# Performance work log

Hardware: AMD Instinct MI355X
Metric: run time of the kernel (lower is better)

The kernel has to match this reference:

```python
import jax, jax.numpy as jnp
import numpy as np

N, E, B = 65536, 131072, 2048
NUM_FEATURES, EDGE_FEATURES, DIM = 75, 16, 64


def setup_inputs() -> dict:
    key = jax.random.key(0)
    ks = jax.random.split(key, 24)

    def p(i, shape, scale=0.05):
        return jax.random.normal(ks[i], shape, dtype=jnp.float32) * scale

    return {
        "node_features": p(0, (N, NUM_FEATURES), 1.0),
        "edge_features": p(1, (E, EDGE_FEATURES), 1.0),
        "edge_index": jax.random.randint(ks[2], (2, E), 0, N),
        "graph_index": jnp.sort(jax.random.randint(ks[3], (N,), 0, B)),
        "lin0_w": p(4, (NUM_FEATURES, DIM)),
        "lin0_b": p(5, (DIM,)),
        "mlp_w1": p(6, (EDGE_FEATURES, 128)),
        "mlp_b1": p(7, (128,)),
        "mlp_w2": p(8, (128, DIM * DIM)),
        "mlp_b2": p(9, (DIM * DIM,)),
        "conv_bias": p(10, (DIM,)),
        "gru_w_ih": p(11, (3 * DIM, DIM)),
        "gru_w_hh": p(12, (3 * DIM, DIM)),
        "gru_b_ih": p(13, (3 * DIM,)),
        "gru_b_hh": p(14, (3 * DIM,)),
        "lstm_w_ih": p(15, (4 * DIM, 2 * DIM)),
        "lstm_w_hh": p(16, (4 * DIM, DIM)),
        "lstm_b_ih": p(17, (4 * DIM,)),
        "lstm_b_hh": p(18, (4 * DIM,)),
    }


def reference(node_features, edge_features, edge_index, graph_index,
              lin0_w, lin0_b, mlp_w1, mlp_b1, mlp_w2, mlp_b2, conv_bias,
              gru_w_ih, gru_w_hh, gru_b_ih, gru_b_hh,
              lstm_w_ih, lstm_w_hh, lstm_b_ih, lstm_b_hh):
    n = node_features.shape[0]
    d = DIM
    src, dst = edge_index[0], edge_index[1]

    # edge-conditioned weights (identical every iteration in the original loop)
    ew = jnp.maximum(edge_features @ mlp_w1 + mlp_b1, 0.0) @ mlp_w2 + mlp_b2
    W = ew.reshape(-1, d, d)  # [E, d, d]
    counts = jnp.maximum(
        jax.ops.segment_sum(jnp.ones(src.shape[0], jnp.float32), dst, num_segments=n), 1.0)

    out = jnp.maximum(node_features @ lin0_w + lin0_b, 0.0)
    h = out
    for _ in range(3):
        # NNConv: gather src, per-edge matmul, scatter-mean to dst
        msg = jnp.einsum('ed,edf->ef', out[src], W)
        agg = jax.ops.segment_sum(msg, dst, num_segments=n) / counts[:, None]
        m = jnp.maximum(agg + conv_bias, 0.0)
        # GRU step (seq len 1)
        gi = m @ gru_w_ih.T + gru_b_ih
        gh = h @ gru_w_hh.T + gru_b_hh
        r = jax.nn.sigmoid(gi[:, :d] + gh[:, :d])
        z = jax.nn.sigmoid(gi[:, d:2 * d] + gh[:, d:2 * d])
        nn_ = jnp.tanh(gi[:, 2 * d:] + r * gh[:, 2 * d:])
        h = (1.0 - z) * nn_ + z * h
        out = h
    feat_map = out

    # Set2Set pooling, 3 processing steps
    q_star = jnp.zeros((B, 2 * d), jnp.float32)
    hs = jnp.zeros((B, d), jnp.float32)
    cs = jnp.zeros((B, d), jnp.float32)
    for _ in range(3):
        gates = q_star @ lstm_w_ih.T + lstm_b_ih + hs @ lstm_w_hh.T + lstm_b_hh
        i_g = jax.nn.sigmoid(gates[:, :d])
        f_g = jax.nn.sigmoid(gates[:, d:2 * d])
        g_g = jnp.tanh(gates[:, 2 * d:3 * d])
        o_g = jax.nn.sigmoid(gates[:, 3 * d:])
        cs = f_g * cs + i_g * g_g
        hs = o_g * jnp.tanh(cs)
        q = hs  # [B, d]
        e = jnp.sum(out * q[graph_index], axis=-1)  # [N]
        e = e - jax.ops.segment_max(e, graph_index, num_segments=B)[graph_index]
        a = jnp.exp(e)
        a = a / (jax.ops.segment_sum(a, graph_index, num_segments=B)[graph_index] + 1e-16)
        rvec = jax.ops.segment_sum(a[:, None] * out, graph_index, num_segments=B)
        q_star = jnp.concatenate([q, rvec], axis=-1)
    return (q_star, feat_map)
```

## Files before the change

### kernel.cpp

```cpp
#include <hip/hip_runtime.h>
#include <hip/hip_bf16.h>

#define GN 65536
#define GE 131072
#define GB 2048

typedef __attribute__((ext_vector_type(8))) short short8;
typedef __attribute__((ext_vector_type(4))) float floatx4;

static __device__ __forceinline__ float sigm(float x) { return 1.0f / (1.0f + __expf(-x)); }
static __device__ __forceinline__ float bf2f(unsigned short u) {
    union { unsigned int i; float f; } v; v.i = ((unsigned int)u) << 16; return v.f;
}
static __device__ __forceinline__ int geti(const void* p, long long i, int f64) {
    return f64 ? (int)((const long long*)p)[i] : ((const int*)p)[i];
}

struct DetectArgs { const void* src[17]; int nhalf[17]; int fi[17]; };
__global__ void k_detect(DetectArgs a, const unsigned int* __restrict__ pe,
                         const unsigned int* __restrict__ pg,
                         int* __restrict__ flags, int* __restrict__ flagE,
                         int* __restrict__ flagG) {
    __shared__ unsigned int sA[256], sB[256];
    if (blockIdx.x >= 17) {
        const unsigned int* p = (blockIdx.x == 17) ? pe : pg;
        const long long nwords = (blockIdx.x == 17) ? (long long)2 * GE : (long long)GN;
        const long long lim = nwords < 16384 ? nwords : 16384;
        unsigned int acc = 0;
        for (long long w = 1 + 2 * (long long)threadIdx.x; w < lim; w += 512) acc |= p[w];
        sA[threadIdx.x] = acc;
        __syncthreads();
        for (int st = 128; st > 0; st >>= 1) {
            if (threadIdx.x < st) sA[threadIdx.x] |= sA[threadIdx.x + st];
            __syncthreads();
        }
        if (threadIdx.x == 0) *((blockIdx.x == 17) ? flagE : flagG) = (sA[0] == 0u) ? 1 : 0;
        return;
    }
    const unsigned short* p = (const unsigned short*)a.src[blockIdx.x];
    const int n0 = a.nhalf[blockIdx.x];
    const int n = n0 < 16384 ? n0 : 16384;
    unsigned int any = 0, orEven = 0;
    for (int i = threadIdx.x; i < n; i += 256) {
        const unsigned short u = p[i];
        const float av = fabsf(bf2f(u));
        if (!(av <= 1e6f)) any = 1u;
        if ((i & 1) == 0) orEven |= u;
    }
    sA[threadIdx.x] = any; sB[threadIdx.x] = orEven;
    __syncthreads();
    for (int s = 128; s > 0; s >>= 1) {
        if (threadIdx.x < s) {
            sA[threadIdx.x] |= sA[threadIdx.x + s];
            sB[threadIdx.x] |= sB[threadIdx.x + s];
        }
        __syncthreads();
    }
    if (threadIdx.x == 0) flags[a.fi[blockIdx.x]] = (sA[0] || sB[0] == 0u) ? 1 : 0;
}

struct CvtArgs { const void* src[15]; float* dst[15]; int n[15]; int fi[15]; int pre[16]; };
__global__ void k_cvt_all(CvtArgs a, const int* __restrict__ flags) {
    const int b = blockIdx.x;
    int t = 0;
    while (t < 14 && b >= a.pre[t + 1]) ++t;
    const int i = (b - a.pre[t]) * 256 + threadIdx.x;
    if (i >= a.n[t]) return;
    const int f = flags[a.fi[t]];
    a.dst[t][i] = f ? ((const float*)a.src[t])[i] : bf2f(((const unsigned short*)a.src[t])[i]);
}

__global__ __launch_bounds__(256) void k_t2(const void* __restrict__ src,
                                            __hip_bfloat16* __restrict__ w2P,
                                            const int* __restrict__ flag) {
    const int tid8 = blockIdx.x * 256 + threadIdx.x;
    const int quad = tid8 & 3, lr = (tid8 >> 2) & 15, rb = (tid8 >> 6) & 7,
              kk = (tid8 >> 9) & 3, t = tid8 >> 11;
    const int n = t * 128 + rb * 16 + lr;
    const int k0 = kk * 32 + quad * 8;
    const int isf32 = *flag;
    short8 v;
    #pragma unroll
    for (int j = 0; j < 8; ++j) {
        const size_t si = (size_t)(k0 + j) * 4096 + n;
        const float f = isf32 ? ((const float*)src)[si] : bf2f(((const unsigned short*)src)[si]);
        const __hip_bfloat16 b = __float2bfloat16(f);
        v[j] = *(const short*)&b;
    }
    *(short8*)(w2P + (size_t)tid8 * 8) = v;
}

__global__ void k_gpack2(const float* __restrict__ w_ih, const float* __restrict__ w_hh,
                         __hip_bfloat16* __restrict__ gwp) {
    const int t = blockIdx.x * 256 + threadIdx.x;
    if (t >= 3072) return;
    const int lane = t & 63;
    const int kk = (t >> 6) & 1;
    const int nb = (t >> 7) % 12;
    const int mat = t / 1536;
    const float* W = mat ? w_hh : w_ih;
    const int c = nb * 16 + (lane & 15);
    const int k0 = kk * 32 + (lane >> 4) * 8;
    short8 hi, lo;
    #pragma unroll
    for (int j = 0; j < 8; ++j) {
        const float v = W[c * 64 + k0 + j];
        const __hip_bfloat16 bh = __float2bfloat16(v);
        hi[j] = *(const short*)&bh;
        const __hip_bfloat16 bl = __float2bfloat16(v - __bfloat162float(bh));
        lo[j] = *(const short*)&bl;
    }
    const size_t base = (size_t)(((mat * 12 + nb) * 2 + kk) * 2);
    *(short8*)(gwp + (base + 0) * 512 + lane * 8) = hi;
    *(short8*)(gwp + (base + 1) * 512 + lane * 8) = lo;
}

__global__ void k_counts(const void* __restrict__ eidx, const int* __restrict__ fi64,
                         float* __restrict__ counts, int E_) {
    int e = blockIdx.x * 256 + threadIdx.x;
    if (e < E_) atomicAdd(&counts[geti(eidx, (long long)E_ + e, *fi64)], 1.0f);
}

__global__ void k_rowptr(const void* __restrict__ gi, const int* __restrict__ fi64,
                         int* __restrict__ rowptr, int N_, int B_) {
    int g = blockIdx.x * 256 + threadIdx.x;
    if (g > B_) return;
    const int f64 = *fi64;
    int lo = 0, hi = N_;
    while (lo < hi) { int mid = (lo + hi) >> 1; if (geti(gi, mid, f64) < g) lo = mid + 1; else hi = mid; }
    rowptr[g] = lo;
}

__global__ __launch_bounds__(256) void k_lin0(const void* __restrict__ nf_raw,
                                              const float* __restrict__ w,
                                              const float* __restrict__ b,
                                              float* __restrict__ out,
                                              const int* __restrict__ flag) {
    const int ln = threadIdx.x >> 6;
    const int d = threadIdx.x & 63;
    const int n = blockIdx.x * 4 + ln;
    const int isf32 = *flag;
    __shared__ float s_nf[4][76];
    const size_t base = (size_t)n * 75;
    s_nf[ln][d] = isf32 ? ((const float*)nf_raw)[base + d] : bf2f(((const unsigned short*)nf_raw)[base + d]);
    if (d < 11) s_nf[ln][64 + d] = isf32 ? ((const float*)nf_raw)[base + 64 + d]
                                         : bf2f(((const unsigned short*)nf_raw)[base + 64 + d]);
    __syncthreads();
    float acc = b[d];
    #pragma unroll
    for (int i = 0; i < 75; ++i) acc += s_nf[ln][i] * w[i * 64 + d];
    out[(size_t)n * 64 + d] = fmaxf(acc, 0.0f);
}

__global__ __launch_bounds__(256) void k1_h1(const void* __restrict__ ef_raw,
                                             const float* __restrict__ w1,
                                             const float* __restrict__ b1,
                                             __hip_bfloat16* __restrict__ h1P,
                                             const int* __restrict__ flag) {
    const int le = threadIdx.x >> 7;
    const int j = threadIdx.x & 127;
    const int e = blockIdx.x * 2 + le;
    const int isf32 = *flag;
    __shared__ float efs[2][16];
    if (j < 16) {
        const size_t idx = (size_t)e * 16 + j;
        efs[le][j] = isf32 ? ((const float*)ef_raw)[idx] : bf2f(((const unsigned short*)ef_raw)[idx]);
    }
    __syncthreads();
    float acc = b1[j];
    #pragma unroll
    for (int i = 0; i < 16; ++i) acc += efs[le][i] * w1[i * 128 + j];
    const int eb = e >> 6, er = e & 63, rb = er >> 4, lre = er & 15;
    const int kk = j >> 5, qd = (j >> 3) & 3, jj = j & 7;
    h1P[(size_t)eb * 8192 + (kk * 4 + rb) * 512 + (qd * 16 + lre) * 8 + jj] =
        __float2bfloat16(fmaxf(acc, 0.0f));
}

__global__ __launch_bounds__(256) void k23_fused(const __hip_bfloat16* __restrict__ h1P,
                                                 const __hip_bfloat16* __restrict__ w2P,
                                                 const float* __restrict__ b2,
                                                 const float* __restrict__ out,
                                                 const void* __restrict__ eidx,
                                                 const int* __restrict__ fi64,
                                                 float* __restrict__ agg) {
    __shared__ __align__(16) __hip_bfloat16 As[64 * 128];
    __shared__ float yT[64][65];
    __shared__ int sdx[64];
    const int tid = threadIdx.x;
    const int e0 = blockIdx.x * 64;
    const int f64 = *fi64;

    const int wave = tid >> 6, lane = tid & 63;
    const int wn = wave * 32;
    const int lr = lane & 15, quad = lane >> 4;

    if (tid < 64) sdx[tid] = geti(eidx, (long long)GE + e0 + tid, f64);
    {
        const short8* s8 = (const short8*)(h1P + (size_t)blockIdx.x * 8192);
        short8* d8 = (short8*)As;
        #pragma unroll
        for (int i = 0; i < 4; ++i) d8[i * 256 + tid] = s8[i * 256 + tid];
    }
    {
        const int e = tid >> 2, d0 = (tid & 3) * 16;
        const int s = geti(eidx, e0 + e, f64);
        const float* srow = out + (size_t)s * 64 + d0;
        #pragma unroll
        for (int j = 0; j < 4; ++j) {
            float4 v = *(const float4*)(srow + j * 4);
            yT[d0 + j * 4 + 0][e] = v.x;
            yT[d0 + j * 4 + 1][e] = v.y;
            yT[d0 + j * 4 + 2][e] = v.z;
            yT[d0 + j * 4 + 3][e] = v.w;
        }
    }
    __syncthreads();

    const int lin = (lr * 4 + quad) * 8;
    const char* Ab = (const char*)As + lane * 16;
    float msum[4][2][4] = {};

#define K23_LOADB(dst, tt)                                                      \
    _Pragma("unroll")                                                           \
    for (int kk = 0; kk < 4; ++kk) {                                            \
        _Pragma("unroll")                                                       \
        for (int nt = 0; nt < 2; ++nt) {                                        \
            const int g = ((tt) * 4 + kk) * 8 + (wn >> 4) + nt;                 \
            dst[kk][nt] = *(const short8*)(w2P + (size_t)g * 512 + lin);        \
        }                                                                       \
    }                                                                           \
    __builtin_amdgcn_sched_barrier(0);

#define K23_BODY(tt, buf) {                                                     \
    const int n0 = (tt) * 128;                                                  \
    const int dcur = (n0 + wn) >> 6;                                            \
    const float b2v0 = b2[n0 + wn + lr];                                        \
    const float b2v1 = b2[n0 + wn + 16 + lr];                                   \
    floatx4 acc[4][2] = {};                                                     \
    _Pragma("unroll")                                                           \
    for (int kk = 0; kk < 4; ++kk) {                                            \
        short8 a0, a1, a2, a3;                                                  \
        a0 = *(const short8*)(Ab + kk * 4096 + 0 * 1024);                       \
        a1 = *(const short8*)(Ab + kk * 4096 + 1 * 1024);                       \
        a2 = *(const short8*)(Ab + kk * 4096 + 2 * 1024);                       \
        a3 = *(const short8*)(Ab + kk * 4096 + 3 * 1024);                       \
        __builtin_amdgcn_s_setprio(1);                                          \
        acc[0][0] = __builtin_amdgcn_mfma_f32_16x16x32_bf16(a0, buf[kk][0], acc[0][0], 0, 0, 0); \
        acc[0][1] = __builtin_amdgcn_mfma_f32_16x16x32_bf16(a0, buf[kk][1], acc[0][1], 0, 0, 0); \
        acc[1][0] = __builtin_amdgcn_mfma_f32_16x16x32_bf16(a1, buf[kk][0], acc[1][0], 0, 0, 0); \
        acc[1][1] = __builtin_amdgcn_mfma_f32_16x16x32_bf16(a1, buf[kk][1], acc[1][1], 0, 0, 0); \
        acc[2][0] = __builtin_amdgcn_mfma_f32_16x16x32_bf16(a2, buf[kk][0], acc[2][0], 0, 0, 0); \
        acc[2][1] = __builtin_amdgcn_mfma_f32_16x16x32_bf16(a2, buf[kk][1], acc[2][1], 0, 0, 0); \
        acc[3][0] = __builtin_amdgcn_mfma_f32_16x16x32_bf16(a3, buf[kk][0], acc[3][0], 0, 0, 0); \
        acc[3][1] = __builtin_amdgcn_mfma_f32_16x16x32_bf16(a3, buf[kk][1], acc[3][1], 0, 0, 0); \
        __builtin_amdgcn_s_setprio(0);                                          \
    }                                                                           \
    _Pragma("unroll")                                                           \
    for (int mt = 0; mt < 4; ++mt) {                                            \
        _Pragma("unroll")                                                       \
        for (int r = 0; r < 4; ++r) {                                           \
            const float yv = yT[dcur][mt * 16 + quad * 4 + r];                  \
            msum[mt][0][r] = fmaf(yv, acc[mt][0][r] + b2v0, msum[mt][0][r]);    \
            msum[mt][1][r] = fmaf(yv, acc[mt][1][r] + b2v1, msum[mt][1][r]);    \
        }                                                                       \
    }                                                                           \
}

    short8 bA[4][2], bB[4][2];
    K23_LOADB(bA, 0)
    #pragma unroll 1
    for (int t = 0; t < 32; t += 2) {
        K23_LOADB(bB, t + 1)
        K23_BODY(t, bA)
        if (t + 2 < 32) { K23_LOADB(bA, t + 2) }
        K23_BODY(t + 1, bB)
    }
#undef K23_LOADB
#undef K23_BODY

    __syncthreads();
    float* mg = (float*)As;
    const int fb = (wn & 32);
    if (wave < 2) {
        #pragma unroll
        for (int mt = 0; mt < 4; ++mt)
            #pragma unroll
            for (int r = 0; r < 4; ++r)
                #pragma unroll
                for (int nt = 0; nt < 2; ++nt)
                    mg[(mt * 16 + quad * 4 + r) * 64 + fb + nt * 16 + lr] = msum[mt][nt][r];
    }
    __syncthreads();
    if (wave >= 2) {
        #pragma unroll
        for (int mt = 0; mt < 4; ++mt)
            #pragma unroll
            for (int r = 0; r < 4; ++r)
                #pragma unroll
                for (int nt = 0; nt < 2; ++nt)
                    mg[(mt * 16 + quad * 4 + r) * 64 + fb + nt * 16 + lr] += msum[mt][nt][r];
    }
    __syncthreads();
    #pragma unroll
    for (int i = 0; i < 16; ++i) {
        const int o = i * 256 + tid;
        const int row = o >> 6, col = o & 63;
        atomicAdd(&agg[(size_t)sdx[row] * 64 + col], mg[o]);
    }
}

__global__ __launch_bounds__(256) void k4_gru(const float* __restrict__ agg,
                                              const float* __restrict__ counts,
                                              const float* __restrict__ cbias,
                                              const __hip_bfloat16* __restrict__ gwp,
                                              const float* __restrict__ b_ih,
                                              const float* __restrict__ b_hh,
                                              float* __restrict__ out) {
    const int wv = threadIdx.x >> 6, lane = threadIdx.x & 63;
    const int lr = lane & 15, quad = lane >> 4;
    const int wnb0 = blockIdx.x * 64 + wv * 16;
    const int node = wnb0 + lr;

    const float rcnt = 1.0f / fmaxf(counts[node], 1.0f);
    const float* ap = agg + (size_t)node * 64;
    const float* hp = out + (size_t)node * 64;
    short8 am[2], ah[2];
    #pragma unroll
    for (int kk = 0; kk < 2; ++kk) {
        const int k0 = kk * 32 + quad * 8;
        #pragma unroll
        for (int j = 0; j < 8; ++j) {
            const float mv = fmaxf(ap[k0 + j] * rcnt + cbias[k0 + j], 0.0f);
            const __hip_bfloat16 mb = __float2bfloat16(mv);
            am[kk][j] = *(const short*)&mb;
            const __hip_bfloat16 hb = __float2bfloat16(hp[k0 + j]);
            ah[kk][j] = *(const short*)&hb;
        }
    }

    floatx4 ai[12] = {}, ahh[12] = {};
    #pragma unroll
    for (int nb = 0; nb < 12; ++nb) {
        #pragma unroll
        for (int kk = 0; kk < 2; ++kk) {
            #pragma unroll
            for (int part = 0; part < 2; ++part) {
                const short8 bi = *(const short8*)(gwp + (size_t)(((0 * 12 + nb) * 2 + kk) * 2 + part) * 512 + lane * 8);
                ai[nb] = __builtin_amdgcn_mfma_f32_16x16x32_bf16(am[kk], bi, ai[nb], 0, 0, 0);
                const short8 bh = *(const short8*)(gwp + (size_t)(((1 * 12 + nb) * 2 + kk) * 2 + part) * 512 + lane * 8);
                ahh[nb] = __builtin_amdgcn_mfma_f32_16x16x32_bf16(ah[kk], bh, ahh[nb], 0, 0, 0);
            }
        }
    }

    #pragma unroll
    for (int f = 0; f < 4; ++f) {
        const int d = f * 16 + lr;
        const float bir = b_ih[d],       bhr = b_hh[d];
        const float biz = b_ih[64 + d],  bhz = b_hh[64 + d];
        const float bin = b_ih[128 + d], bhn = b_hh[128 + d];
        #pragma unroll
        for (int r = 0; r < 4; ++r) {
            const int row = wnb0 + quad * 4 + r;
            const float rr = sigm(ai[f][r] + bir + ahh[f][r] + bhr);
            const float zz = sigm(ai[f + 4][r] + biz + ahh[f + 4][r] + bhz);
            const float nn = tanhf(ai[f + 8][r] + bin + rr * (ahh[f + 8][r] + bhn));
            const float hd = out[(size_t)row * 64 + d];
            out[(size_t)row * 64 + d] = (1.0f - zz) * nn + zz * hd;
        }
    }
}

__global__ __launch_bounds__(256) void k5_fused(float* __restrict__ qstar,
                                                const float* __restrict__ w_ih,
                                                const float* __restrict__ w_hh,
                                                const float* __restrict__ b_ih,
                                                const float* __restrict__ b_hh,
                                                const float* __restrict__ out,
                                                const int* __restrict__ rowptr) {
    const int g = blockIdx.x;
    const int j = threadIdx.x;
    __shared__ float qs[128], hv[64], gates[256];
    __shared__ float smw[4], sSw[4], srw[4][64];
    if (j < 128) qs[j] = 0.0f;
    if (j < 64) hv[j] = 0.0f;
    float creg = 0.0f;
    const int wv = j >> 6, lane = j & 63;
    const int start = rowptr[g], end = rowptr[g + 1];
    const float bsum = b_ih[j] + b_hh[j];

    for (int step = 0; step < 3; ++step) {
        __syncthreads();
        float acc = bsum;
        for (int k4 = 0; k4 < 128; k4 += 4) {
            float4 v = *(const float4*)(w_ih + (size_t)j * 128 + k4);
            const float* pv = (const float*)&v;
            #pragma unroll
            for (int t = 0; t < 4; ++t) acc += qs[k4 + t] * pv[t];
        }
        for (int k4 = 0; k4 < 64; k4 += 4) {
            float4 v = *(const float4*)(w_hh + (size_t)j * 64 + k4);
            const float* pv = (const float*)&v;
            #pragma unroll
            for (int t = 0; t < 4; ++t) acc += hv[k4 + t] * pv[t];
        }
        gates[j] = acc;
        __syncthreads();
        if (j < 64) {
            const float ig = sigm(gates[j]);
            const float fg = sigm(gates[64 + j]);
            const float gg = tanhf(gates[128 + j]);
            const float og = sigm(gates[192 + j]);
            creg = fg * creg + ig * gg;
            const float h = og * tanhf(creg);
            hv[j] = h;
            qs[j] = h;
        }
        __syncthreads();
        const float q = hv[lane];
        float m = -3.4e38f, S = 0.0f, racc = 0.0f;
        for (int n = start + wv; n < end; n += 4) {
            const float ov = out[(size_t)n * 64 + lane];
            float p = ov * q;
            #pragma unroll
            for (int off = 1; off < 64; off <<= 1) p += __shfl_xor(p, off);
            if (p > m) {
                const float sc = __expf(m - p);
                S = S * sc + 1.0f;
                racc = racc * sc + ov;
                m = p;
            } else {
                const float w = __expf(p - m);
                S += w;
                racc += w * ov;
            }
        }
        if (lane == 0) { smw[wv] = m; sSw[wv] = S; }
        srw[wv][lane] = racc;
        __syncthreads();
        if (wv == 0) {
            const float mstar = fmaxf(fmaxf(smw[0], smw[1]), fmaxf(smw[2], smw[3]));
            float Ssum = 0.0f, rsum = 0.0f;
            #pragma unroll
            for (int i = 0; i < 4; ++i) {
                const float sc = __expf(smw[i] - mstar);
                Ssum += sSw[i] * sc;
                rsum += srw[i][lane] * sc;
            }
            qs[64 + lane] = rsum / (Ssum + 1e-16f);
        }
    }
    __syncthreads();
    if (j < 128) qstar[(size_t)g * 128 + j] = qs[j];
}

__global__ void k_out(const float* __restrict__ qstar, const float* __restrict__ outb,
                      float* __restrict__ dst, int nq, int nfeat, int out_n) {
    int i = blockIdx.x * 256 + threadIdx.x;
    if (i >= out_n) return;
    float v = 0.0f;
    if (i < nq) v = qstar[i];
    else if (i - nq < nfeat) v = outb[i - nq];
    dst[i] = v;
}

extern "C" void kernel_launch(void* const* d_in, const int* in_sizes, int n_in,
                              void* d_out, int out_size, void* d_ws, size_t ws_size,
                              hipStream_t stream) {
    constexpr int N = GN, E = GE, B = GB;

    char* ws = (char*)d_ws;
    size_t off = 0;
    auto alloc = [&](size_t bytes) { size_t o = off; off = (off + bytes + 255) & ~(size_t)255; return o; };

    int*   fl     = (int*)  (ws + alloc(19 * 4));
    int*   flagE  = (int*)  (ws + alloc(256));
    int*   flagG  = (int*)  (ws + alloc(256));
    float* counts = (float*)(ws + alloc((size_t)N * 4));
    int*   rowptr = (int*)  (ws + alloc((size_t)(B + 1) * 4));
    float* outbuf = (float*)(ws + alloc((size_t)N * 64 * 4));
    float* agg    = (float*)(ws + alloc((size_t)N * 64 * 4));
    float* qstar  = (float*)(ws + alloc((size_t)B * 128 * 4));
    __hip_bfloat16* h1  = (__hip_bfloat16*)(ws + alloc((size_t)E * 128 * 2));
    __hip_bfloat16* w2P = (__hip_bfloat16*)(ws + alloc((size_t)4096 * 128 * 2));
    __hip_bfloat16* gwp = (__hip_bfloat16*)(ws + alloc((size_t)2 * 12 * 2 * 2 * 512 * 2));

    const int fidx[15]  = {4, 5, 6, 7, 8, 9, 10, 11, 12, 13, 14, 15, 16, 17, 18};
    const int fsize[15] = {75 * 64, 64, 16 * 128, 128, 128 * 4096, 4096, 64,
                           192 * 64, 192 * 64, 192, 192, 256 * 128, 256 * 64, 256, 256};
    float* F[19] = {};
    for (int t = 0; t < 15; ++t) F[fidx[t]] = (float*)(ws + alloc((size_t)fsize[t] * 4));

    DetectArgs da;
    da.src[0] = d_in[0]; da.nhalf[0] = N * 75; da.fi[0] = 0;
    da.src[1] = d_in[1]; da.nhalf[1] = E * 16; da.fi[1] = 1;
    for (int t = 0; t < 15; ++t) { da.src[2 + t] = d_in[fidx[t]]; da.nhalf[2 + t] = fsize[t]; da.fi[2 + t] = fidx[t]; }
    k_detect<<<19, 256, 0, stream>>>(da, (const unsigned int*)d_in[2],
                                     (const unsigned int*)d_in[3], fl, flagE, flagG);

    CvtArgs ca;
    int pre = 0;
    for (int t = 0; t < 15; ++t) {
        ca.src[t] = d_in[fidx[t]]; ca.dst[t] = F[fidx[t]]; ca.n[t] = fsize[t]; ca.fi[t] = fidx[t];
        ca.pre[t] = pre; pre += (fsize[t] + 255) / 256;
    }
    ca.pre[15] = pre;
    k_cvt_all<<<pre, 256, 0, stream>>>(ca, fl);
    k_t2<<<256, 256, 0, stream>>>(d_in[8], w2P, fl + 8);
    k_gpack2<<<12, 256, 0, stream>>>(F[11], F[12], gwp);

    hipMemsetAsync(counts, 0, (size_t)N * 4, stream);
    hipMemsetAsync(qstar, 0, (size_t)B * 128 * 4, stream);

    k_counts<<<E / 256, 256, 0, stream>>>(d_in[2], flagE, counts, E);
    k_rowptr<<<(B + 1 + 255) / 256, 256, 0, stream>>>(d_in[3], flagG, rowptr, N, B);
    k_lin0<<<N / 4, 256, 0, stream>>>(d_in[0], F[4], F[5], outbuf, fl + 0);
    k1_h1<<<E / 2, 256, 0, stream>>>(d_in[1], F[6], F[7], h1, fl + 1);

    for (int it = 0; it < 3; ++it) {
        hipMemsetAsync(agg, 0, (size_t)N * 64 * 4, stream);
        k23_fused<<<E / 64, 256, 0, stream>>>(h1, w2P, F[9], outbuf, d_in[2], flagE, agg);
        k4_gru<<<N / 64, 256, 0, stream>>>(agg, counts, F[10], gwp, F[13], F[14], outbuf);
    }
    k5_fused<<<B, 256, 0, stream>>>(qstar, F[15], F[16], F[17], F[18], outbuf, rowptr);
    k_out<<<(out_size + 255) / 256, 256, 0, stream>>>(qstar, outbuf, (float*)d_out,
                                                      B * 128, N * 64, out_size);
}
```

Before: 970.9 us.

## Merge setup kernels, batch lin0/h1 per block, fold agg zeroing into GRU

Combines the counts and rowptr kernels into one launch. lin0 now processes 16 nodes per block with the weight matrix staged in shared memory, and h1 processes 16 edges per block with weight columns held in registers. The per-iteration agg memset is replaced by having the GRU kernel zero agg after reading it, and k23_fused gets a launch-bounds occupancy hint. The conversion of mlp_w2 is removed from the generic conversion pass, since it is handled by the transpose kernel. Together these aim to cut launch count, redundant weight loads and memset traffic, at the cost of GRU doing extra stores.

```diff
diff --git a/kernel.cpp b/kernel.cpp
--- a/kernel.cpp
+++ b/kernel.cpp
@@ -115,18 +115,18 @@
     *(short8*)(gwp + (base + 1) * 512 + lane * 8) = lo;
 }
 
-__global__ void k_counts(const void* __restrict__ eidx, const int* __restrict__ fi64,
-                         float* __restrict__ counts, int E_) {
-    int e = blockIdx.x * 256 + threadIdx.x;
-    if (e < E_) atomicAdd(&counts[geti(eidx, (long long)E_ + e, *fi64)], 1.0f);
-}
-
-__global__ void k_rowptr(const void* __restrict__ gi, const int* __restrict__ fi64,
-                         int* __restrict__ rowptr, int N_, int B_) {
-    int g = blockIdx.x * 256 + threadIdx.x;
-    if (g > B_) return;
-    const int f64 = *fi64;
-    int lo = 0, hi = N_;
+__global__ void k_cnt_rp(const void* __restrict__ eidx, const void* __restrict__ gi,
+                         const int* __restrict__ flagE, const int* __restrict__ flagG,
+                         float* __restrict__ counts, int* __restrict__ rowptr) {
+    if (blockIdx.x < 512) {
+        const int e = blockIdx.x * 256 + threadIdx.x;
+        atomicAdd(&counts[geti(eidx, (long long)GE + e, *flagE)], 1.0f);
+        return;
+    }
+    const int g = (blockIdx.x - 512) * 256 + threadIdx.x;
+    if (g > GB) return;
+    const int f64 = *flagG;
+    int lo = 0, hi = GN;
     while (lo < hi) { int mid = (lo + hi) >> 1; if (geti(gi, mid, f64) < g) lo = mid + 1; else hi = mid; }
     rowptr[g] = lo;
 }
@@ -136,20 +136,28 @@
                                               const float* __restrict__ b,
                                               float* __restrict__ out,
                                               const int* __restrict__ flag) {
-    const int ln = threadIdx.x >> 6;
-    const int d = threadIdx.x & 63;
-    const int n = blockIdx.x * 4 + ln;
+    __shared__ float sw[75][66];
+    __shared__ float snf[16][76];
+    const int tid = threadIdx.x;
     const int isf32 = *flag;
-    __shared__ float s_nf[4][76];
-    const size_t base = (size_t)n * 75;
-    s_nf[ln][d] = isf32 ? ((const float*)nf_raw)[base + d] : bf2f(((const unsigned short*)nf_raw)[base + d]);
-    if (d < 11) s_nf[ln][64 + d] = isf32 ? ((const float*)nf_raw)[base + 64 + d]
-                                         : bf2f(((const unsigned short*)nf_raw)[base + 64 + d]);
-    __syncthreads();
-    float acc = b[d];
-    #pragma unroll
-    for (int i = 0; i < 75; ++i) acc += s_nf[ln][i] * w[i * 64 + d];
-    out[(size_t)n * 64 + d] = fmaxf(acc, 0.0f);
+    const int nb0 = blockIdx.x * 16;
+    for (int i = tid; i < 75 * 64; i += 256) sw[i >> 6][i & 63] = w[i];
+    for (int i = tid; i < 16 * 75; i += 256) {
+        const int nn = i / 75, ii = i % 75;
+        const size_t idx = (size_t)(nb0 + nn) * 75 + ii;
+        snf[nn][ii] = isf32 ? ((const float*)nf_raw)[idx] : bf2f(((const unsigned short*)nf_raw)[idx]);
+    }
+    __syncthreads();
+    const int ln = tid >> 6, d = tid & 63;
+    const float bd = b[d];
+    #pragma unroll
+    for (int g = 0; g < 4; ++g) {
+        const int nn = ln * 4 + g;
+        float acc = bd;
+        #pragma unroll
+        for (int i = 0; i < 75; ++i) acc = fmaf(snf[nn][i], sw[i][d], acc);
+        out[(size_t)(nb0 + nn) * 64 + d] = fmaxf(acc, 0.0f);
+    }
 }
 
 __global__ __launch_bounds__(256) void k1_h1(const void* __restrict__ ef_raw,
@@ -157,26 +165,34 @@
                                              const float* __restrict__ b1,
                                              __hip_bfloat16* __restrict__ h1P,
                                              const int* __restrict__ flag) {
-    const int le = threadIdx.x >> 7;
-    const int j = threadIdx.x & 127;
-    const int e = blockIdx.x * 2 + le;
+    const int j = threadIdx.x & 127, half = threadIdx.x >> 7;
+    const int eb0 = blockIdx.x * 16;
     const int isf32 = *flag;
-    __shared__ float efs[2][16];
-    if (j < 16) {
-        const size_t idx = (size_t)e * 16 + j;
-        efs[le][j] = isf32 ? ((const float*)ef_raw)[idx] : bf2f(((const unsigned short*)ef_raw)[idx]);
-    }
-    __syncthreads();
-    float acc = b1[j];
-    #pragma unroll
-    for (int i = 0; i < 16; ++i) acc += efs[le][i] * w1[i * 128 + j];
-    const int eb = e >> 6, er = e & 63, rb = er >> 4, lre = er & 15;
+    __shared__ float efs[16][17];
+    {
+        const int e = threadIdx.x >> 4, i = threadIdx.x & 15;
+        const size_t idx = (size_t)(eb0 + e) * 16 + i;
+        efs[e][i] = isf32 ? ((const float*)ef_raw)[idx] : bf2f(((const unsigned short*)ef_raw)[idx]);
+    }
+    __syncthreads();
+    float wcol[16];
+    #pragma unroll
+    for (int i = 0; i < 16; ++i) wcol[i] = w1[i * 128 + j];
+    const float bj = b1[j];
     const int kk = j >> 5, qd = (j >> 3) & 3, jj = j & 7;
-    h1P[(size_t)eb * 8192 + (kk * 4 + rb) * 512 + (qd * 16 + lre) * 8 + jj] =
-        __float2bfloat16(fmaxf(acc, 0.0f));
-}
-
-__global__ __launch_bounds__(256) void k23_fused(const __hip_bfloat16* __restrict__ h1P,
+    #pragma unroll
+    for (int eo = 0; eo < 8; ++eo) {
+        const int e = eb0 + half * 8 + eo;
+        float acc = bj;
+        #pragma unroll
+        for (int i = 0; i < 16; ++i) acc = fmaf(efs[half * 8 + eo][i], wcol[i], acc);
+        const int ebk = e >> 6, er = e & 63, rb = er >> 4, lre = er & 15;
+        h1P[(size_t)ebk * 8192 + (kk * 4 + rb) * 512 + (qd * 16 + lre) * 8 + jj] =
+            __float2bfloat16(fmaxf(acc, 0.0f));
+    }
+}
+
+__global__ __launch_bounds__(256, 3) void k23_fused(const __hip_bfloat16* __restrict__ h1P,
                                                  const __hip_bfloat16* __restrict__ w2P,
                                                  const float* __restrict__ b2,
                                                  const float* __restrict__ out,
@@ -309,7 +325,7 @@
     }
 }
 
-__global__ __launch_bounds__(256) void k4_gru(const float* __restrict__ agg,
+__global__ __launch_bounds__(256) void k4_gru(float* __restrict__ agg,
                                               const float* __restrict__ counts,
                                               const float* __restrict__ cbias,
                                               const __hip_bfloat16* __restrict__ gwp,
@@ -322,7 +338,7 @@
     const int node = wnb0 + lr;
 
     const float rcnt = 1.0f / fmaxf(counts[node], 1.0f);
-    const float* ap = agg + (size_t)node * 64;
+    float* ap = agg + (size_t)node * 64;
     const float* hp = out + (size_t)node * 64;
     short8 am[2], ah[2];
     #pragma unroll
@@ -335,6 +351,15 @@
             am[kk][j] = *(const short*)&mb;
             const __hip_bfloat16 hb = __float2bfloat16(hp[k0 + j]);
             ah[kk][j] = *(const short*)&hb;
+        }
+    }
+    {
+        const float4 z = {0.0f, 0.0f, 0.0f, 0.0f};
+        #pragma unroll
+        for (int kk = 0; kk < 2; ++kk) {
+            const int k0 = kk * 32 + quad * 8;
+            *(float4*)(ap + k0) = z;
+            *(float4*)(ap + k0 + 4) = z;
         }
     }
 
@@ -481,7 +506,7 @@
     float* outbuf = (float*)(ws + alloc((size_t)N * 64 * 4));
     float* agg    = (float*)(ws + alloc((size_t)N * 64 * 4));
     float* qstar  = (float*)(ws + alloc((size_t)B * 128 * 4));
-    __hip_bfloat16* h1  = (__hip_bfloat16*)(ws + alloc((size_t)E * 128 * 2));
+    __hip_bfloat16* h1P = (__hip_bfloat16*)(ws + alloc((size_t)E * 128 * 2));
     __hip_bfloat16* w2P = (__hip_bfloat16*)(ws + alloc((size_t)4096 * 128 * 2));
     __hip_bfloat16* gwp = (__hip_bfloat16*)(ws + alloc((size_t)2 * 12 * 2 * 2 * 512 * 2));
 
@@ -498,28 +523,32 @@
     k_detect<<<19, 256, 0, stream>>>(da, (const unsigned int*)d_in[2],
                                      (const unsigned int*)d_in[3], fl, flagE, flagG);
 
+    const int cidx[14]  = {4, 5, 6, 7, 9, 10, 11, 12, 13, 14, 15, 16, 17, 18};
+    const int csize[14] = {75 * 64, 64, 16 * 128, 128, 4096, 64,
+                           192 * 64, 192 * 64, 192, 192, 256 * 128, 256 * 64, 256, 256};
     CvtArgs ca;
     int pre = 0;
-    for (int t = 0; t < 15; ++t) {
-        ca.src[t] = d_in[fidx[t]]; ca.dst[t] = F[fidx[t]]; ca.n[t] = fsize[t]; ca.fi[t] = fidx[t];
-        ca.pre[t] = pre; pre += (fsize[t] + 255) / 256;
-    }
-    ca.pre[15] = pre;
+    for (int t = 0; t < 14; ++t) {
+        ca.src[t] = d_in[cidx[t]]; ca.dst[t] = F[cidx[t]]; ca.n[t] = csize[t]; ca.fi[t] = cidx[t];
+        ca.pre[t] = pre; pre += (csize[t] + 255) / 256;
+    }
+    ca.src[14] = d_in[4]; ca.dst[14] = F[4]; ca.n[14] = 0; ca.fi[14] = 4;
+    ca.pre[14] = pre; ca.pre[15] = pre;
     k_cvt_all<<<pre, 256, 0, stream>>>(ca, fl);
     k_t2<<<256, 256, 0, stream>>>(d_in[8], w2P, fl + 8);
     k_gpack2<<<12, 256, 0, stream>>>(F[11], F[12], gwp);
 
     hipMemsetAsync(counts, 0, (size_t)N * 4, stream);
     hipMemsetAsync(qstar, 0, (size_t)B * 128 * 4, stream);
-
-    k_counts<<<E / 256, 256, 0, stream>>>(d_in[2], flagE, counts, E);
-    k_rowptr<<<(B + 1 + 255) / 256, 256, 0, stream>>>(d_in[3], flagG, rowptr, N, B);
-    k_lin0<<<N / 4, 256, 0, stream>>>(d_in[0], F[4], F[5], outbuf, fl + 0);
-    k1_h1<<<E / 2, 256, 0, stream>>>(d_in[1], F[6], F[7], h1, fl + 1);
+    hipMemsetAsync(agg, 0, (size_t)N * 64 * 4, stream);
+
+    k_cnt_rp<<<512 + (B + 1 + 255) / 256, 256, 0, stream>>>(d_in[2], d_in[3], flagE, flagG,
+                                                            counts, rowptr);
+    k_lin0<<<N / 16, 256, 0, stream>>>(d_in[0], F[4], F[5], outbuf, fl + 0);
+    k1_h1<<<E / 16, 256, 0, stream>>>(d_in[1], F[6], F[7], h1P, fl + 1);
 
     for (int it = 0; it < 3; ++it) {
-        hipMemsetAsync(agg, 0, (size_t)N * 64 * 4, stream);
-        k23_fused<<<E / 64, 256, 0, stream>>>(h1, w2P, F[9], outbuf, d_in[2], flagE, agg);
+        k23_fused<<<E / 64, 256, 0, stream>>>(h1P, w2P, F[9], outbuf, d_in[2], flagE, agg);
         k4_gru<<<N / 64, 256, 0, stream>>>(agg, counts, F[10], gwp, F[13], F[14], outbuf);
     }
     k5_fused<<<B, 256, 0, stream>>>(qstar, F[15], F[16], F[17], F[18], outbuf, rowptr);
```

Result: faster. 876.0 us (-9.8%).
